# Kernel optimization log

Hardware: AMD Instinct MI355X
Metric: run time of the kernel (lower is better)

## Reference

```python
import math
import jax, jax.numpy as jnp
import numpy as np

B = 128          # graphs per batch
N = 1024         # nodes per graph
E = 1048576      # total edges (avg degree 8)
F_IN = 64
NHID = 64
NCLS = 10
RATIO = 0.8


def setup_inputs() -> dict:
    key = jax.random.key(0)
    ks = jax.random.split(key, 24)
    x = jax.random.normal(ks[0], (B * N, F_IN), jnp.float32)
    # intra-graph random edges: graph id per edge, local src/dst
    epg = E // B
    gid = jnp.repeat(jnp.arange(B, dtype=jnp.int32), epg)
    src = gid * N + jax.random.randint(ks[1], (E,), 0, N, jnp.int32)
    dst = gid * N + jax.random.randint(ks[2], (E,), 0, N, jnp.int32)
    def lin(k, fi, fo):
        s = 1.0 / np.sqrt(fi)
        return jax.random.uniform(k, (fi, fo), jnp.float32, -s, s)
    p = {
        'W1': lin(ks[3], F_IN, NHID), 'b1': jnp.zeros((NHID,), jnp.float32),
        'Wp1': lin(ks[4], NHID, 1), 'bp1': jnp.zeros((1,), jnp.float32),
        'W2': lin(ks[5], NHID, NHID), 'b2': jnp.zeros((NHID,), jnp.float32),
        'Wp2': lin(ks[6], NHID, 1), 'bp2': jnp.zeros((1,), jnp.float32),
        'W3': lin(ks[7], NHID, NHID), 'b3': jnp.zeros((NHID,), jnp.float32),
        'Wp3': lin(ks[8], NHID, 1), 'bp3': jnp.zeros((1,), jnp.float32),
        'L1w': lin(ks[9], 2 * NHID, NHID), 'L1b': jnp.zeros((NHID,), jnp.float32),
        'L2w': lin(ks[10], NHID, NHID // 2), 'L2b': jnp.zeros((NHID // 2,), jnp.float32),
        'L3w': lin(ks[11], NHID // 2, NCLS), 'L3b': jnp.zeros((NCLS,), jnp.float32),
    }
    return dict(x=x, edge_src=src, edge_dst=dst, **p)


def gcn_conv(x, W, b, src, dst, emask, n):
    # PyG GCNConv: add self loops, symmetric deg normalization
    xw = x @ W
    ew = emask.astype(x.dtype)
    deg = jax.ops.segment_sum(ew, dst, num_segments=n) + 1.0  # +1 self loop
    dis = jax.lax.rsqrt(deg)
    norm = dis[src] * dis[dst] * ew
    agg = jax.ops.segment_sum(xw[src] * norm[:, None], dst, num_segments=n)
    agg = agg + xw * (dis * dis)[:, None]  # self-loop message
    return agg + b


def sag_pool(x, Wp, bp, src, dst, emask, n_cur):
    n_tot = B * n_cur
    k = int(math.ceil(RATIO * n_cur))
    score = gcn_conv(x, Wp, bp, src, dst, emask, n_tot)[:, 0]
    _, idx = jax.lax.top_k(score.reshape(B, n_cur), k)
    perm = (idx + (jnp.arange(B, dtype=jnp.int32) * n_cur)[:, None]).reshape(-1)
    xn = x[perm] * jnp.tanh(score[perm])[:, None]
    new_idx = jnp.full((n_tot,), -1, jnp.int32).at[perm].set(
        jnp.arange(B * k, dtype=jnp.int32))
    ns, nd = new_idx[src], new_idx[dst]
    valid = emask & (ns >= 0) & (nd >= 0)
    return xn, jnp.where(valid, ns, 0), jnp.where(valid, nd, 0), valid, k


def readout(x, k):
    xr = x.reshape(B, k, NHID)
    return jnp.concatenate([xr.max(axis=1), xr.mean(axis=1)], axis=1)


def reference(x, edge_src, edge_dst, W1, b1, Wp1, bp1, W2, b2, Wp2, bp2,
              W3, b3, Wp3, bp3, L1w, L1b, L2w, L2b, L3w, L3b):
    src = edge_src.astype(jnp.int32)
    dst = edge_dst.astype(jnp.int32)
    emask = jnp.ones((E,), bool)
    n = N
    h = jax.nn.relu(gcn_conv(x, W1, b1, src, dst, emask, B * n))
    h, src, dst, emask, n = sag_pool(h, Wp1, bp1, src, dst, emask, n)
    r1 = readout(h, n)
    h = jax.nn.relu(gcn_conv(h, W2, b2, src, dst, emask, B * n))
    h, src, dst, emask, n = sag_pool(h, Wp2, bp2, src, dst, emask, n)
    r2 = readout(h, n)
    h = jax.nn.relu(gcn_conv(h, W3, b3, src, dst, emask, B * n))
    h, src, dst, emask, n = sag_pool(h, Wp3, bp3, src, dst, emask, n)
    r3 = readout(h, n)
    z = r1 + r2 + r3
    z = jax.nn.relu(z @ L1w + L1b)          # dropout is identity in eval
    z = jax.nn.relu(z @ L2w + L2b)
    return jax.nn.log_softmax(z @ L3w + L3b, axis=-1)
```

## Files before the change

kernel.cpp:

```cpp
#include <hip/hip_runtime.h>
#include <math.h>

constexpr int B_  = 128;
constexpr int N_  = 1024;
constexpr int E_  = 1048576;
constexpr int BN_ = B_ * N_;
constexpr int EPG = E_ / B_;
constexpr int NSEG = 16;

typedef short v8s __attribute__((ext_vector_type(8)));
typedef float v4f __attribute__((ext_vector_type(4)));

__device__ __forceinline__ unsigned bf16_rne(unsigned u) {
    return (u + 0x7FFFu + ((u >> 16) & 1u)) >> 16;
}

__global__ __launch_bounds__(1024) void k_csr2(
        const int* __restrict__ src, const int* __restrict__ dst,
        const int* __restrict__ cum,
        int* __restrict__ srt, int* __restrict__ rowptr,
        float* __restrict__ dis, int n) {
    __shared__ int cnt[1024];
    __shared__ int cur[1024];
    __shared__ int cums[1024];
    __shared__ int wsum[17];
    int g = blockIdx.x, tid = threadIdx.x;
    int gb   = g * N_;
    int base = g * n;
    const int eb = g * EPG;

    cums[tid] = cum ? cum[gb + tid] : tid;
    cnt[tid] = 0;
    __syncthreads();
    for (int t = tid; t < EPG; t += 1024) {
        int s = cums[src[eb + t] - gb];
        int d = cums[dst[eb + t] - gb];
        if ((s | d) >= 0) atomicAdd(&cnt[d], 1);
    }
    __syncthreads();

    int c = (tid < n) ? cnt[tid] : 0;
    int v = c;
    int lane = tid & 63, wv = tid >> 6;
    #pragma unroll
    for (int off = 1; off < 64; off <<= 1) {
        int t = __shfl_up(v, off, 64);
        if (lane >= off) v += t;
    }
    if (lane == 63) wsum[wv] = v;
    __syncthreads();
    if (tid == 0) {
        int run = 0;
        #pragma unroll
        for (int i = 0; i < 16; ++i) { int t = wsum[i]; wsum[i] = run; run += t; }
        wsum[16] = run;
    }
    __syncthreads();
    int excl = v - c + wsum[wv];
    if (tid < n) {
        cur[tid] = excl;
        rowptr[g * (n + 1) + tid] = excl;
        dis[base + tid] = rsqrtf((float)c + 1.0f);
    }
    if (tid == 0) rowptr[g * (n + 1) + n] = wsum[16];
    __syncthreads();

    for (int t = tid; t < EPG; t += 1024) {
        int s = cums[src[eb + t] - gb];
        int d = cums[dst[eb + t] - gb];
        if ((s | d) < 0) continue;
        int pos = atomicAdd(&cur[d], 1);
        srt[eb + pos] = s;
    }
}

__global__ __launch_bounds__(1024) void k_wprep3(
        const float* __restrict__ W0, const float* __restrict__ W1,
        const float* __restrict__ W2, unsigned short* __restrict__ wfall) {
    const float* W = (blockIdx.x == 0) ? W0 : (blockIdx.x == 1) ? W1 : W2;
    unsigned short* wf = wfall + (size_t)blockIdx.x * 8192;
    int t = threadIdx.x;
    int l  = t & 63;
    int kk = (t >> 6) & 1;
    int c  = (t >> 7) & 3;
    int p  = (t >> 9) & 1;
    int col = c * 16 + (l & 15);
    int kbase = kk * 32 + (l >> 4) * 8;
    unsigned short o[8];
    #pragma unroll
    for (int j = 0; j < 8; ++j) {
        float w = W[(kbase + j) * 64 + col];
        unsigned u  = __float_as_uint(w);
        unsigned hi = bf16_rne(u);
        if (p == 0) o[j] = (unsigned short)hi;
        else {
            float lo = w - __uint_as_float(hi << 16);
            o[j] = (unsigned short)bf16_rne(__float_as_uint(lo));
        }
    }
    uint4 v;
    v.x = o[0] | ((unsigned)o[1] << 16);
    v.y = o[2] | ((unsigned)o[3] << 16);
    v.z = o[4] | ((unsigned)o[5] << 16);
    v.w = o[6] | ((unsigned)o[7] << 16);
    *reinterpret_cast<uint4*>(wf + (size_t)t * 8) = v;
}

__global__ __launch_bounds__(256) void k_xw_mfma(
        const float* __restrict__ h, const int* __restrict__ perm,
        const float* __restrict__ ggate, const unsigned short* __restrict__ wf,
        const float* __restrict__ dis, float* __restrict__ xwq, int rows) {
    __shared__ float hs[128][68];
    __shared__ float sdis[128];
    __shared__ int   lperm[128];
    __shared__ float lgate[128];
    int tid = threadIdx.x;
    int r0 = blockIdx.x * 128;

    if (perm) {
        if (tid < 128) { lperm[tid] = perm[r0 + tid]; lgate[tid] = ggate[r0 + tid]; }
        __syncthreads();
        for (int i = tid; i < 128 * 16; i += 256) {
            int row = i >> 4, s = i & 15;
            float4 v = *reinterpret_cast<const float4*>(h + (size_t)lperm[row] * 64 + s * 4);
            float gt = lgate[row];
            v.x *= gt; v.y *= gt; v.z *= gt; v.w *= gt;
            *reinterpret_cast<float4*>(&hs[row][s * 4]) = v;
        }
    } else {
        for (int i = tid; i < 128 * 16; i += 256) {
            int row = i >> 4, s = i & 15;
            float4 v = *reinterpret_cast<const float4*>(h + (size_t)(r0 + row) * 64 + s * 4);
            *reinterpret_cast<float4*>(&hs[row][s * 4]) = v;
        }
    }
    if (tid < 128) sdis[tid] = dis[r0 + tid];

    int lane = tid & 63;
    v8s wh[4][2], wl[4][2];
    #pragma unroll
    for (int c = 0; c < 4; ++c) {
        #pragma unroll
        for (int kk = 0; kk < 2; ++kk) {
            wh[c][kk] = *reinterpret_cast<const v8s*>(wf + (((size_t)((0*4 + c)*2 + kk))*64 + lane)*8);
            wl[c][kk] = *reinterpret_cast<const v8s*>(wf + (((size_t)((1*4 + c)*2 + kk))*64 + lane)*8);
        }
    }
    __syncthreads();

    int wave = tid >> 6;
    int m = lane & 15, b = lane >> 4;
    #pragma unroll
    for (int t = 0; t < 2; ++t) {
        int lr0 = (wave * 2 + t) * 16;
        float f[16];
        *reinterpret_cast<float4*>(f)      = *reinterpret_cast<const float4*>(&hs[lr0 + m][b * 8]);
        *reinterpret_cast<float4*>(f + 4)  = *reinterpret_cast<const float4*>(&hs[lr0 + m][b * 8 + 4]);
        *reinterpret_cast<float4*>(f + 8)  = *reinterpret_cast<const float4*>(&hs[lr0 + m][32 + b * 8]);
        *reinterpret_cast<float4*>(f + 12) = *reinterpret_cast<const float4*>(&hs[lr0 + m][32 + b * 8 + 4]);
        v8s ah[2], al[2];
        #pragma unroll
        for (int ch = 0; ch < 2; ++ch) {
            #pragma unroll
            for (int j = 0; j < 8; ++j) {
                float x = f[ch * 8 + j];
                unsigned u  = __float_as_uint(x);
                unsigned hi = bf16_rne(u);
                float lo = x - __uint_as_float(hi << 16);
                ah[ch][j] = (short)hi;
                al[ch][j] = (short)bf16_rne(__float_as_uint(lo));
            }
        }
        float dv[4];
        #pragma unroll
        for (int reg = 0; reg < 4; ++reg) dv[reg] = sdis[lr0 + b * 4 + reg];

        #pragma unroll
        for (int c = 0; c < 4; ++c) {
            v4f acc = {0.f, 0.f, 0.f, 0.f};
            acc = __builtin_amdgcn_mfma_f32_16x16x32_bf16(ah[0], wh[c][0], acc, 0, 0, 0);
            acc = __builtin_amdgcn_mfma_f32_16x16x32_bf16(ah[1], wh[c][1], acc, 0, 0, 0);
            acc = __builtin_amdgcn_mfma_f32_16x16x32_bf16(al[0], wh[c][0], acc, 0, 0, 0);
            acc = __builtin_amdgcn_mfma_f32_16x16x32_bf16(al[1], wh[c][1], acc, 0, 0, 0);
            acc = __builtin_amdgcn_mfma_f32_16x16x32_bf16(ah[0], wl[c][0], acc, 0, 0, 0);
            acc = __builtin_amdgcn_mfma_f32_16x16x32_bf16(ah[1], wl[c][1], acc, 0, 0, 0);
            acc = __builtin_amdgcn_mfma_f32_16x16x32_bf16(al[0], wl[c][0], acc, 0, 0, 0);
            acc = __builtin_amdgcn_mfma_f32_16x16x32_bf16(al[1], wl[c][1], acc, 0, 0, 0);
            #pragma unroll
            for (int reg = 0; reg < 4; ++reg) {
                int grow = r0 + lr0 + b * 4 + reg;
                xwq[((size_t)c * rows + grow) * 16 + m] = acc[reg] * dv[reg];
            }
        }
    }
}

__global__ __launch_bounds__(1024) void k_agg_csr(
        const int* __restrict__ srt, const int* __restrict__ rowptr,
        const float* __restrict__ dis, const float* __restrict__ xwq,
        const float* __restrict__ bias, const float* __restrict__ Wp,
        float* __restrict__ hout, float* __restrict__ sxwsq,
        int n, int rows) {
    extern __shared__ float lds[];
    float* xs  = lds;
    int* lsrt  = (int*)(lds + n * 20);
    int* lrp   = lsrt + EPG;
    int g = blockIdx.x >> 2, q = blockIdx.x & 3;
    int foff = q * 16;
    int tid  = threadIdx.x;
    int base = g * n;
    const float* plane = xwq + ((size_t)q * rows + base) * 16;

    for (int i = tid; i < n * 4; i += 1024) {
        int row = i >> 2, sub = i & 3;
        float4 v = *reinterpret_cast<const float4*>(plane + row * 16 + sub * 4);
        *reinterpret_cast<float4*>(xs + row * 20 + sub * 4) = v;
    }
    for (int i = tid; i <= n; i += 1024) lrp[i] = rowptr[g * (n + 1) + i];
    __syncthreads();
    int total = lrp[n];
    const int* gsrt = srt + g * EPG;
    for (int i = tid; i < total; i += 1024) lsrt[i] = gsrt[i];
    __syncthreads();

    int sub = tid & 3;
    float4 b   = *reinterpret_cast<const float4*>(bias + foff + sub * 4);
    float4 wp4 = *reinterpret_cast<const float4*>(Wp   + foff + sub * 4);
    for (int row = tid >> 2; row < n; row += 256) {
        int s0 = lrp[row], s1 = lrp[row + 1];
        float4 acc = *reinterpret_cast<const float4*>(xs + row * 20 + sub * 4);
        for (int j = s0; j < s1; ++j) {
            int s = lsrt[j];
            const float4 v = *reinterpret_cast<const float4*>(xs + s * 20 + sub * 4);
            acc.x += v.x; acc.y += v.y; acc.z += v.z; acc.w += v.w;
        }
        float dsc = dis[base + row];
        float4 o;
        o.x = fmaxf(fmaf(dsc, acc.x, b.x), 0.0f);
        o.y = fmaxf(fmaf(dsc, acc.y, b.y), 0.0f);
        o.z = fmaxf(fmaf(dsc, acc.z, b.z), 0.0f);
        o.w = fmaxf(fmaf(dsc, acc.w, b.w), 0.0f);
        *reinterpret_cast<float4*>(hout + (size_t)(base + row) * 64 + foff + sub * 4) = o;
        float part = o.x * wp4.x + o.y * wp4.y + o.z * wp4.z + o.w * wp4.w;
        part += __shfl_xor(part, 1, 64);
        part += __shfl_xor(part, 2, 64);
        if (sub == 0) sxwsq[(size_t)q * BN_ + base + row] = part;
    }
}

__global__ __launch_bounds__(1024) void k_score_topk(
        const int* __restrict__ srt, const int* __restrict__ rowptr,
        const float* __restrict__ dis, const float* __restrict__ sxwsq,
        const float* __restrict__ bp, int n, int k,
        int* __restrict__ perm, float* __restrict__ ggate,
        int* __restrict__ cum, int do_compose) {
    __shared__ float xs[1024];
    __shared__ int   lrp[1025];
    __shared__ int   lsrt[EPG];
    unsigned long long* keys = (unsigned long long*)lsrt;
    int* mark = (int*)xs;
    int g = blockIdx.x, tid = threadIdx.x;
    int base = g * n;
    float bp0 = bp[0];

    if (tid < n) {
        float s0 = sxwsq[0 * (size_t)BN_ + base + tid] + sxwsq[1 * (size_t)BN_ + base + tid]
                 + sxwsq[2 * (size_t)BN_ + base + tid] + sxwsq[3 * (size_t)BN_ + base + tid];
        xs[tid] = s0 * dis[base + tid];
    }
    for (int i = tid; i <= n; i += 1024) lrp[i] = rowptr[g * (n + 1) + i];
    __syncthreads();
    int total = lrp[n];
    for (int i = tid; i < total; i += 1024) lsrt[i] = srt[g * EPG + i];
    __syncthreads();

    float sag = 0.0f;
    if (tid < n) {
        float acc = xs[tid];
        int s1 = lrp[tid + 1];
        for (int j = lrp[tid]; j < s1; ++j) acc += xs[lsrt[j]];
        sag = dis[base + tid] * acc + bp0;
    }
    __syncthreads();

    {
        unsigned long long kv = 0ull;
        if (tid < n) {
            unsigned u  = __float_as_uint(sag);
            unsigned mk = (u & 0x80000000u) ? ~u : (u | 0x80000000u);
            kv = ((unsigned long long)mk << 32) | (unsigned)tid;
        }
        keys[tid] = kv;
        mark[tid] = -1;
    }

    for (int size = 2; size <= 1024; size <<= 1) {
        for (int stride = size >> 1; stride > 0; stride >>= 1) {
            __syncthreads();
            if (tid < 512) {
                int a  = ((tid / stride) * (stride << 1)) + (tid & (stride - 1));
                int bx = a + stride;
                bool asc = ((a & size) == 0);
                unsigned long long ka = keys[a], kb = keys[bx];
                bool sw = asc ? (ka > kb) : (ka < kb);
                if (sw) { keys[a] = kb; keys[bx] = ka; }
            }
        }
    }
    __syncthreads();

    if (tid < k) {
        int j = tid;
        unsigned long long kv = keys[1023 - j];
        int local   = (int)(kv & 0xFFFFFFFFull);
        unsigned mk = (unsigned)(kv >> 32);
        unsigned u  = (mk & 0x80000000u) ? (mk ^ 0x80000000u) : ~mk;
        int newg = g * k + j;
        perm[newg]  = base + local;
        ggate[newg] = tanhf(__uint_as_float(u));
        mark[local] = j;
    }
    __syncthreads();
    if (do_compose) {
        int gb = g * N_;
        int c = (do_compose == 1) ? tid : cum[gb + tid];
        cum[gb + tid] = (c >= 0) ? mark[c] : -1;
    }
}

__global__ __launch_bounds__(256) void k_readout_seg(
        const float* __restrict__ h, const int* __restrict__ perm,
        const float* __restrict__ ggate, int k, float* __restrict__ pz) {
    int g = blockIdx.x / NSEG, seg = blockIdx.x % NSEG;
    int ck = (k + NSEG - 1) / NSEG;
    int j0 = seg * ck;
    int j1 = min(k, j0 + ck);
    __shared__ float gate[64];
    __shared__ int   lperm[64];
    int tid = threadIdx.x;
    for (int j = j0 + tid; j < j1; j += 256) {
        lperm[j - j0] = perm[g * k + j];
        gate[j - j0]  = ggate[g * k + j];
    }
    __syncthreads();
    int lane = tid & 63, w = tid >> 6;
    float mx = -INFINITY, sm = 0.0f;
    for (int j = j0 + w; j < j1; j += 4) {
        float v = h[(size_t)lperm[j - j0] * 64 + lane] * gate[j - j0];
        mx = fmaxf(mx, v); sm += v;
    }
    __shared__ float smx[4][64], ssm[4][64];
    smx[w][lane] = mx; ssm[w][lane] = sm;
    __syncthreads();
    if (w == 0) {
        #pragma unroll
        for (int i = 1; i < 4; ++i) { mx = fmaxf(mx, smx[i][lane]); sm += ssm[i][lane]; }
        float* p = pz + ((size_t)g * NSEG + seg) * 128;
        p[lane]      = mx;
        p[64 + lane] = sm;
    }
}

__global__ __launch_bounds__(128) void k_mlp(const float* __restrict__ pz,
                      const float* __restrict__ L1w, const float* __restrict__ L1b,
                      const float* __restrict__ L2w, const float* __restrict__ L2b,
                      const float* __restrict__ L3w, const float* __restrict__ L3b,
                      float* __restrict__ out) {
    __shared__ float z[128], h1[64], h2[32], lg[10], lse;
    int g = blockIdx.x, tid = threadIdx.x;
    const float kinv[3] = {1.0f / 820.0f, 1.0f / 656.0f, 1.0f / 525.0f};
    float zv = 0.0f;
    if (tid < 64) {
        #pragma unroll
        for (int L = 0; L < 3; ++L) {
            const float* p = pz + (((size_t)L * B_ + g) * NSEG) * 128;
            float mx = -INFINITY;
            #pragma unroll
            for (int s = 0; s < NSEG; ++s) mx = fmaxf(mx, p[s * 128 + tid]);
            zv += mx;
        }
    } else {
        int f = tid - 64;
        #pragma unroll
        for (int L = 0; L < 3; ++L) {
            const float* p = pz + (((size_t)L * B_ + g) * NSEG) * 128;
            float sm = 0.0f;
            #pragma unroll
            for (int s = 0; s < NSEG; ++s) sm += p[s * 128 + 64 + f];
            zv += sm * kinv[L];
        }
    }
    z[tid] = zv;
    __syncthreads();
    if (tid < 64) {
        float acc = L1b[tid];
        for (int i = 0; i < 128; ++i) acc = fmaf(z[i], L1w[i * 64 + tid], acc);
        h1[tid] = fmaxf(acc, 0.0f);
    }
    __syncthreads();
    if (tid < 32) {
        float acc = L2b[tid];
        for (int i = 0; i < 64; ++i) acc = fmaf(h1[i], L2w[i * 32 + tid], acc);
        h2[tid] = fmaxf(acc, 0.0f);
    }
    __syncthreads();
    if (tid < 10) {
        float acc = L3b[tid];
        for (int i = 0; i < 32; ++i) acc = fmaf(h2[i], L3w[i * 10 + tid], acc);
        lg[tid] = acc;
    }
    __syncthreads();
    if (tid == 0) {
        float m = lg[0];
        for (int i = 1; i < 10; ++i) m = fmaxf(m, lg[i]);
        float s = 0.0f;
        for (int i = 0; i < 10; ++i) s += expf(lg[i] - m);
        lse = m + logf(s);
    }
    __syncthreads();
    if (tid < 10) out[g * 10 + tid] = lg[tid] - lse;
}

extern "C" void kernel_launch(void* const* d_in, const int* in_sizes, int n_in,
                              void* d_out, int out_size, void* d_ws, size_t ws_size,
                              hipStream_t stream) {
    const float* x    = (const float*)d_in[0];
    const int*   esrc = (const int*)d_in[1];
    const int*   edst = (const int*)d_in[2];
    const float* W [3] = {(const float*)d_in[3],  (const float*)d_in[7],  (const float*)d_in[11]};
    const float* bb[3] = {(const float*)d_in[4],  (const float*)d_in[8],  (const float*)d_in[12]};
    const float* Wp[3] = {(const float*)d_in[5],  (const float*)d_in[9],  (const float*)d_in[13]};
    const float* bp[3] = {(const float*)d_in[6],  (const float*)d_in[10], (const float*)d_in[14]};
    const float* L1w = (const float*)d_in[15];
    const float* L1b = (const float*)d_in[16];
    const float* L2w = (const float*)d_in[17];
    const float* L2b = (const float*)d_in[18];
    const float* L3w = (const float*)d_in[19];
    const float* L3b = (const float*)d_in[20];
    float* out = (float*)d_out;

    float* fws   = (float*)d_ws;
    float* xwq   = fws;
    float* agg   = xwq  + (size_t)BN_ * 64;
    float* dis   = agg  + (size_t)BN_ * 64;
    float* sxwsq = dis  + BN_;
    float* ggate = sxwsq + 4 * (size_t)BN_;
    float* pz    = ggate + BN_;
    int*   perm   = (int*)(pz + 3 * B_ * NSEG * 128);
    int*   cum    = perm + BN_;
    int*   srt    = cum + BN_;
    int*   rowptr = srt + E_;
    unsigned short* wfrag = (unsigned short*)(rowptr + B_ * (N_ + 1));

    hipFuncSetAttribute(reinterpret_cast<const void*>(k_agg_csr),
                        hipFuncAttributeMaxDynamicSharedMemorySize,
                        (1024 * 20 + EPG + 1025) * 4);

    k_wprep3<<<3, 1024, 0, stream>>>(W[0], W[1], W[2], wfrag);

    const int ks_[3] = {820, 656, 525};
    int n = N_;

    for (int L = 0; L < 3; ++L) {
        int rows = B_ * n;
        int k    = ks_[L];

        k_csr2<<<B_, 1024, 0, stream>>>(esrc, edst, (L == 0) ? nullptr : cum,
                                        srt, rowptr, dis, n);

        if (L == 0)
            k_xw_mfma<<<rows / 128, 256, 0, stream>>>(x, nullptr, nullptr,
                                                      wfrag, dis, xwq, rows);
        else
            k_xw_mfma<<<rows / 128, 256, 0, stream>>>(agg, perm, ggate,
                                                      wfrag + (size_t)L * 8192, dis, xwq, rows);

        k_agg_csr<<<B_ * 4, 1024, (size_t)(n * 20 + EPG + n + 1) * 4, stream>>>(
            srt, rowptr, dis, xwq, bb[L], Wp[L], agg, sxwsq, n, rows);

        k_score_topk<<<B_, 1024, 0, stream>>>(srt, rowptr, dis, sxwsq, bp[L], n, k,
                                              perm, ggate, cum, (L < 2) ? (L + 1) : 0);

        k_readout_seg<<<B_ * NSEG, 256, 0, stream>>>(agg, perm, ggate, k,
                                                     pz + (size_t)L * B_ * NSEG * 128);

        n = k;
    }

    k_mlp<<<B_, 128, 0, stream>>>(pz, L1w, L1b, L2w, L2b, L3w, L3b, out);
}
```

Measured before the change: 227.0 us.

## Pad CSR rows to multiples of four and fuse score aggregation into agg kernel

Each CSR row is padded to a multiple of four entries, and the padding points to a zero dummy node. The agg kernel can then gather neighbours four at a time with int4 index loads. The SAG score aggregation now runs inside k_agg_csr on the per-quarter partial dot products already held in LDS, so k_score_topk no longer reloads the edge list and rowptr and only sums four partials before the bitonic top-k. Blocks are also reordered to be quarter-major. The cost is extra padding writes in the CSR build, a larger srt buffer, and a second LDS pass in the agg kernel.

After: 262.1 us. +15.5%, slower.

```diff
diff --git a/kernel.cpp b/kernel.cpp
--- a/kernel.cpp
+++ b/kernel.cpp
@@ -1,11 +1,12 @@
 #include <hip/hip_runtime.h>
 #include <math.h>
 
-constexpr int B_  = 128;
-constexpr int N_  = 1024;
-constexpr int E_  = 1048576;
-constexpr int BN_ = B_ * N_;
-constexpr int EPG = E_ / B_;
+constexpr int B_   = 128;
+constexpr int N_   = 1024;
+constexpr int E_   = 1048576;
+constexpr int BN_  = B_ * N_;
+constexpr int EPG  = E_ / B_;
+constexpr int SRT2 = EPG + 3 * 1024;
 constexpr int NSEG = 16;
 
 typedef short v8s __attribute__((ext_vector_type(8)));
@@ -28,6 +29,7 @@
     int gb   = g * N_;
     int base = g * n;
     const int eb = g * EPG;
+    int* gsrt = srt + (size_t)g * SRT2;
 
     cums[tid] = cum ? cum[gb + tid] : tid;
     cnt[tid] = 0;
@@ -39,8 +41,9 @@
     }
     __syncthreads();
 
-    int c = (tid < n) ? cnt[tid] : 0;
-    int v = c;
+    int c  = (tid < n) ? cnt[tid] : 0;
+    int pc = (c + 3) & ~3;
+    int v = pc;
     int lane = tid & 63, wv = tid >> 6;
     #pragma unroll
     for (int off = 1; off < 64; off <<= 1) {
@@ -56,7 +59,7 @@
         wsum[16] = run;
     }
     __syncthreads();
-    int excl = v - c + wsum[wv];
+    int excl = v - pc + wsum[wv];
     if (tid < n) {
         cur[tid] = excl;
         rowptr[g * (n + 1) + tid] = excl;
@@ -70,7 +73,13 @@
         int d = cums[dst[eb + t] - gb];
         if ((s | d) < 0) continue;
         int pos = atomicAdd(&cur[d], 1);
-        srt[eb + pos] = s;
+        gsrt[pos] = s;
+    }
+    __syncthreads();
+
+    if (tid < n) {
+        int e1 = excl + pc;
+        for (int t = cur[tid]; t < e1; ++t) gsrt[t] = n;
     }
 }
 
@@ -195,17 +204,18 @@
     }
 }
 
-__global__ __launch_bounds__(1024) void k_agg_csr(
+__global__ __launch_bounds__(1024, 1) void k_agg_csr(
         const int* __restrict__ srt, const int* __restrict__ rowptr,
         const float* __restrict__ dis, const float* __restrict__ xwq,
         const float* __restrict__ bias, const float* __restrict__ Wp,
-        float* __restrict__ hout, float* __restrict__ sxwsq,
+        float* __restrict__ hout, float* __restrict__ saggq,
         int n, int rows) {
-    extern __shared__ float lds[];
-    float* xs  = lds;
-    int* lsrt  = (int*)(lds + n * 20);
-    int* lrp   = lsrt + EPG;
-    int g = blockIdx.x >> 2, q = blockIdx.x & 3;
+    extern __shared__ float xs[];
+    int lrpPad = (n + 4) & ~3;
+    int* lrp  = (int*)(xs + (n + 1) * 20);
+    int* lsrt = lrp + lrpPad;
+
+    int g = blockIdx.x & 127, q = blockIdx.x >> 7;
     int foff = q * 16;
     int tid  = threadIdx.x;
     int base = g * n;
@@ -216,83 +226,79 @@
         float4 v = *reinterpret_cast<const float4*>(plane + row * 16 + sub * 4);
         *reinterpret_cast<float4*>(xs + row * 20 + sub * 4) = v;
     }
+    if (tid < 20) xs[n * 20 + tid] = 0.0f;
     for (int i = tid; i <= n; i += 1024) lrp[i] = rowptr[g * (n + 1) + i];
     __syncthreads();
     int total = lrp[n];
-    const int* gsrt = srt + g * EPG;
+    const int* gsrt = srt + (size_t)g * SRT2;
     for (int i = tid; i < total; i += 1024) lsrt[i] = gsrt[i];
     __syncthreads();
 
     int sub = tid & 3;
-    float4 b   = *reinterpret_cast<const float4*>(bias + foff + sub * 4);
+    float4 bq  = *reinterpret_cast<const float4*>(bias + foff + sub * 4);
     float4 wp4 = *reinterpret_cast<const float4*>(Wp   + foff + sub * 4);
     for (int row = tid >> 2; row < n; row += 256) {
         int s0 = lrp[row], s1 = lrp[row + 1];
         float4 acc = *reinterpret_cast<const float4*>(xs + row * 20 + sub * 4);
-        for (int j = s0; j < s1; ++j) {
-            int s = lsrt[j];
-            const float4 v = *reinterpret_cast<const float4*>(xs + s * 20 + sub * 4);
-            acc.x += v.x; acc.y += v.y; acc.z += v.z; acc.w += v.w;
+        for (int j = s0; j < s1; j += 4) {
+            int4 nb = *reinterpret_cast<const int4*>(lsrt + j);
+            const float4 v0 = *reinterpret_cast<const float4*>(xs + nb.x * 20 + sub * 4);
+            const float4 v1 = *reinterpret_cast<const float4*>(xs + nb.y * 20 + sub * 4);
+            const float4 v2 = *reinterpret_cast<const float4*>(xs + nb.z * 20 + sub * 4);
+            const float4 v3 = *reinterpret_cast<const float4*>(xs + nb.w * 20 + sub * 4);
+            acc.x += v0.x + v1.x + v2.x + v3.x;
+            acc.y += v0.y + v1.y + v2.y + v3.y;
+            acc.z += v0.z + v1.z + v2.z + v3.z;
+            acc.w += v0.w + v1.w + v2.w + v3.w;
         }
         float dsc = dis[base + row];
         float4 o;
-        o.x = fmaxf(fmaf(dsc, acc.x, b.x), 0.0f);
-        o.y = fmaxf(fmaf(dsc, acc.y, b.y), 0.0f);
-        o.z = fmaxf(fmaf(dsc, acc.z, b.z), 0.0f);
-        o.w = fmaxf(fmaf(dsc, acc.w, b.w), 0.0f);
+        o.x = fmaxf(fmaf(dsc, acc.x, bq.x), 0.0f);
+        o.y = fmaxf(fmaf(dsc, acc.y, bq.y), 0.0f);
+        o.z = fmaxf(fmaf(dsc, acc.z, bq.z), 0.0f);
+        o.w = fmaxf(fmaf(dsc, acc.w, bq.w), 0.0f);
         *reinterpret_cast<float4*>(hout + (size_t)(base + row) * 64 + foff + sub * 4) = o;
         float part = o.x * wp4.x + o.y * wp4.y + o.z * wp4.z + o.w * wp4.w;
         part += __shfl_xor(part, 1, 64);
         part += __shfl_xor(part, 2, 64);
-        if (sub == 0) sxwsq[(size_t)q * BN_ + base + row] = part;
+        if (sub == 0) xs[row * 20 + 16] = part * dsc;
+    }
+    __syncthreads();
+
+    for (int row = tid; row < n; row += 1024) {
+        float acc = xs[row * 20 + 16];
+        int s1 = lrp[row + 1];
+        for (int j = lrp[row]; j < s1; j += 4) {
+            int4 nb = *reinterpret_cast<const int4*>(lsrt + j);
+            acc += xs[nb.x * 20 + 16] + xs[nb.y * 20 + 16]
+                 + xs[nb.z * 20 + 16] + xs[nb.w * 20 + 16];
+        }
+        saggq[(size_t)q * BN_ + base + row] = acc;
     }
 }
 
 __global__ __launch_bounds__(1024) void k_score_topk(
-        const int* __restrict__ srt, const int* __restrict__ rowptr,
-        const float* __restrict__ dis, const float* __restrict__ sxwsq,
+        const float* __restrict__ dis, const float* __restrict__ saggq,
         const float* __restrict__ bp, int n, int k,
         int* __restrict__ perm, float* __restrict__ ggate,
         int* __restrict__ cum, int do_compose) {
-    __shared__ float xs[1024];
-    __shared__ int   lrp[1025];
-    __shared__ int   lsrt[EPG];
-    unsigned long long* keys = (unsigned long long*)lsrt;
-    int* mark = (int*)xs;
+    __shared__ unsigned long long keys[1024];
+    __shared__ int mark[1024];
     int g = blockIdx.x, tid = threadIdx.x;
     int base = g * n;
     float bp0 = bp[0];
 
+    unsigned long long kv = 0ull;
     if (tid < n) {
-        float s0 = sxwsq[0 * (size_t)BN_ + base + tid] + sxwsq[1 * (size_t)BN_ + base + tid]
-                 + sxwsq[2 * (size_t)BN_ + base + tid] + sxwsq[3 * (size_t)BN_ + base + tid];
-        xs[tid] = s0 * dis[base + tid];
-    }
-    for (int i = tid; i <= n; i += 1024) lrp[i] = rowptr[g * (n + 1) + i];
-    __syncthreads();
-    int total = lrp[n];
-    for (int i = tid; i < total; i += 1024) lsrt[i] = srt[g * EPG + i];
-    __syncthreads();
-
-    float sag = 0.0f;
-    if (tid < n) {
-        float acc = xs[tid];
-        int s1 = lrp[tid + 1];
-        for (int j = lrp[tid]; j < s1; ++j) acc += xs[lsrt[j]];
-        sag = dis[base + tid] * acc + bp0;
-    }
-    __syncthreads();
-
-    {
-        unsigned long long kv = 0ull;
-        if (tid < n) {
-            unsigned u  = __float_as_uint(sag);
-            unsigned mk = (u & 0x80000000u) ? ~u : (u | 0x80000000u);
-            kv = ((unsigned long long)mk << 32) | (unsigned)tid;
-        }
-        keys[tid] = kv;
-        mark[tid] = -1;
-    }
+        float s0 = saggq[0 * (size_t)BN_ + base + tid] + saggq[1 * (size_t)BN_ + base + tid]
+                 + saggq[2 * (size_t)BN_ + base + tid] + saggq[3 * (size_t)BN_ + base + tid];
+        float sag = dis[base + tid] * s0 + bp0;
+        unsigned u  = __float_as_uint(sag);
+        unsigned mk = (u & 0x80000000u) ? ~u : (u | 0x80000000u);
+        kv = ((unsigned long long)mk << 32) | (unsigned)tid;
+    }
+    keys[tid] = kv;
+    mark[tid] = -1;
 
     for (int size = 2; size <= 1024; size <<= 1) {
         for (int stride = size >> 1; stride > 0; stride >>= 1) {
@@ -311,9 +317,9 @@
 
     if (tid < k) {
         int j = tid;
-        unsigned long long kv = keys[1023 - j];
-        int local   = (int)(kv & 0xFFFFFFFFull);
-        unsigned mk = (unsigned)(kv >> 32);
+        unsigned long long kvv = keys[1023 - j];
+        int local   = (int)(kvv & 0xFFFFFFFFull);
+        unsigned mk = (unsigned)(kvv >> 32);
         unsigned u  = (mk & 0x80000000u) ? (mk ^ 0x80000000u) : ~mk;
         int newg = g * k + j;
         perm[newg]  = base + local;
@@ -440,21 +446,21 @@
     float* out = (float*)d_out;
 
     float* fws   = (float*)d_ws;
-    float* xwq   = fws;
-    float* agg   = xwq  + (size_t)BN_ * 64;
-    float* dis   = agg  + (size_t)BN_ * 64;
-    float* sxwsq = dis  + BN_;
-    float* ggate = sxwsq + 4 * (size_t)BN_;
+    float* agg   = fws;
+    float* xwq   = agg  + (size_t)BN_ * 64;
+    float* dis   = xwq  + (size_t)BN_ * 64;
+    float* saggq = dis  + BN_;
+    float* ggate = saggq + 4 * (size_t)BN_;
     float* pz    = ggate + BN_;
     int*   perm   = (int*)(pz + 3 * B_ * NSEG * 128);
     int*   cum    = perm + BN_;
     int*   srt    = cum + BN_;
-    int*   rowptr = srt + E_;
+    int*   rowptr = srt + (size_t)B_ * SRT2;
     unsigned short* wfrag = (unsigned short*)(rowptr + B_ * (N_ + 1));
 
     hipFuncSetAttribute(reinterpret_cast<const void*>(k_agg_csr),
                         hipFuncAttributeMaxDynamicSharedMemorySize,
-                        (1024 * 20 + EPG + 1025) * 4);
+                        (1025 * 20 + 1028 + SRT2) * 4);
 
     k_wprep3<<<3, 1024, 0, stream>>>(W[0], W[1], W[2], wfrag);
 
@@ -475,10 +481,11 @@
             k_xw_mfma<<<rows / 128, 256, 0, stream>>>(agg, perm, ggate,
                                                       wfrag + (size_t)L * 8192, dis, xwq, rows);
 
-        k_agg_csr<<<B_ * 4, 1024, (size_t)(n * 20 + EPG + n + 1) * 4, stream>>>(
-            srt, rowptr, dis, xwq, bb[L], Wp[L], agg, sxwsq, n, rows);
-
-        k_score_topk<<<B_, 1024, 0, stream>>>(srt, rowptr, dis, sxwsq, bp[L], n, k,
+        int lrpPad = (n + 4) & ~3;
+        k_agg_csr<<<B_ * 4, 1024, (size_t)((n + 1) * 20 + lrpPad + SRT2) * 4, stream>>>(
+            srt, rowptr, dis, xwq, bb[L], Wp[L], agg, saggq, n, rows);
+
+        k_score_topk<<<B_, 1024, 0, stream>>>(dis, saggq, bp[L], n, k,
                                               perm, ggate, cum, (L < 2) ? (L + 1) : 0);
 
         k_readout_seg<<<B_ * NSEG, 256, 0, stream>>>(agg, perm, ggate, k,
```
